# Kernel optimization log

Hardware: AMD Instinct MI355X
Metric: run time of the kernel (lower is better)

The kernel has to match this reference:

```python
import jax, jax.numpy as jnp
import numpy as np

B, N, C, H = 1, 256, 128, 4
DH = C // H  # per-head dim = 32
KEY_SCALE = DH ** -0.5


def setup_inputs() -> dict:
    key = jax.random.key(0)
    ks = jax.random.split(key, 9)
    return {
        "q_data": jax.random.normal(ks[0], (B, N, N, C), jnp.float32),
        "m_data": jax.random.normal(ks[1], (B, N, N, C), jnp.float32),
        "bias": jax.random.normal(ks[2], (B, N, 1, 1, N), jnp.float32),
        "nonbatched_bias": jax.random.normal(ks[3], (1, H, N, N), jnp.float32),
        "wq": jax.random.normal(ks[4], (C, C), jnp.float32) * (1.0 / np.sqrt(C)),
        "wk": jax.random.normal(ks[5], (C, C), jnp.float32) * (1.0 / np.sqrt(C)),
        "wv": jax.random.normal(ks[6], (C, C), jnp.float32) * (1.0 / np.sqrt(C)),
        "wo": jax.random.normal(ks[7], (C, C), jnp.float32) * (1.0 / np.sqrt(C)),
        "bo": jnp.zeros((C,), jnp.float32),
        "wg": jax.random.normal(ks[8], (C, C), jnp.float32) * (1.0 / np.sqrt(C)),
        "bg": jnp.ones((C,), jnp.float32),
    }


def reference(q_data, m_data, bias, nonbatched_bias, wq, wk, wv, wo, bo, wg, bg):
    # projections (torch Linear: x @ W.T), weights stored [out, in]
    q = (q_data @ wq.T) * KEY_SCALE            # [B, N, Nq, H*DH]
    k = m_data @ wk.T                          # [B, N, Nk, H*DH]
    v = m_data @ wv.T                          # [B, N, Nk, H*DH]
    q = q.reshape(B, N, N, H, DH)
    k = k.reshape(B, N, N, H, DH)
    v = v.reshape(B, N, N, H, DH)
    # logits: [B, N, H, Nq, Nk]
    logits = jnp.einsum("bnqhd,bnkhd->bnhqk", q, k)
    logits = logits + bias + nonbatched_bias   # bias [B,N,1,1,Nk]; nb [1,H,Nq,Nk]
    weight = jax.nn.softmax(logits, axis=-1)
    wa = jnp.einsum("bnhqk,bnkhd->bnqhd", weight, v)  # [B, N, Nq, H, DH]
    g = jax.nn.sigmoid(q_data @ wg.T + bg).reshape(B, N, N, H, DH)
    wa = wa * g
    out = wa.reshape(B, N, N, H * DH) @ wo.T + bo
    return out
```

## Files before the change

### kernel.cpp

```cpp
#include <hip/hip_runtime.h>
#include <hip/hip_bf16.h>

typedef unsigned short u16;
typedef unsigned int u32;

#define N_ 256
#define C_ 128
#define H_ 4
#define DH_ 32
#define R_ (N_*N_)

static constexpr float KEY_SCALE_ = 0.17677669529663687f;
static constexpr float LOG2E_ = 1.4426950408889634f;

typedef __attribute__((ext_vector_type(8))) short bf16x8;
typedef __attribute__((ext_vector_type(4))) float f32x4;

__device__ __forceinline__ float bf2f(u16 b){ return __uint_as_float(((u32)b)<<16); }
__device__ __forceinline__ u16 f2bf(float f){
  __hip_bfloat16 h = __float2bfloat16(f);
  u16 r; __builtin_memcpy(&r, &h, 2); return r;
}
__device__ __forceinline__ u32 pack2bf(float lo, float hi){
  __hip_bfloat162 h2 = __float22bfloat162_rn(make_float2(lo, hi));
  u32 r; __builtin_memcpy(&r, &h2, 4); return r;
}

__global__ __launch_bounds__(256) void prep_kernel(
    const float* __restrict__ wq, const float* __restrict__ wk,
    const float* __restrict__ wv, const float* __restrict__ wg,
    const float* __restrict__ nb,
    u16* __restrict__ wtb, float* __restrict__ nbT)
{
  __shared__ float T[64][65];
  const int b = blockIdx.x;
  const int t = threadIdx.x;
  if (b < 64){
    int id = b*256 + t;
    int m = id >> 12;
    int e = (id & 4095)*4;
    const float* src = (m==0) ? wq : (m==1) ? wk : (m==2) ? wv : wg;
    const float4 v = *(const float4*)(src + e);
    const float s = (m==0) ? KEY_SCALE_*LOG2E_ : 1.f;
    uint2 o;
    o.x = pack2bf(v.x*s, v.y*s);
    o.y = pack2bf(v.z*s, v.w*s);
    *(uint2*)(wtb + m*16384 + e) = o;
  } else {
    const int bb = b - 64;
    const int q0 = (bb & 3)*64, k0 = ((bb >> 2) & 3)*64;
    const int h = bb >> 4;
    const float* src = nb + (size_t)h*N_*N_;
    float* dst = nbT + (size_t)h*N_*N_;
    #pragma unroll
    for (int p=0;p<16;p++){
      int id = t + p*256;
      int r = id >> 6, cc = id & 63;
      T[cc][r] = src[(size_t)(q0 + r)*N_ + k0 + cc];
    }
    __syncthreads();
    #pragma unroll
    for (int p=0;p<16;p++){
      int id = t + p*256;
      int r = id >> 6, cc = id & 63;
      dst[(size_t)(k0 + r)*N_ + q0 + cc] = T[r][cc] * LOG2E_;
    }
  }
}

#define XSTR 136
__global__ __launch_bounds__(256, 2) void proj_kernel(
    const float* __restrict__ qd, const float* __restrict__ md,
    const u16* __restrict__ wtb, const float* __restrict__ bg,
    u16* __restrict__ qb, u16* __restrict__ kb,
    u16* __restrict__ vb, u16* __restrict__ gb)
{
  __shared__ u16 Xs[128*XSTR];
  const int t = threadIdx.x;
  const int y = blockIdx.y;
  const size_t row0 = (size_t)blockIdx.x * 128;
  const float* X = y ? md : qd;

  #pragma unroll
  for (int p=0;p<8;p++){
    int id = t + p*256;
    int r = id >> 4, c0 = (id & 15)*8;
    const float* s = X + (row0 + r)*C_ + c0;
    float4 a = *(const float4*)s;
    float4 b = *(const float4*)(s+4);
    uint2 w0; w0.x = pack2bf(a.x, a.y); w0.y = pack2bf(a.z, a.w);
    uint2 w1; w1.x = pack2bf(b.x, b.y); w1.y = pack2bf(b.z, b.w);
    *(uint2*)&Xs[r*XSTR + c0]     = w0;
    *(uint2*)&Xs[r*XSTR + c0 + 4] = w1;
  }

  const int w = t >> 6, l = t & 63, c = l & 15, g = l >> 4;
  const int matSel = w >> 1;
  const int oh = w & 1;
  const int matIdx = y ? (matSel ? 2 : 1) : (matSel ? 3 : 0);
  u16* dst = y ? (matSel ? vb : kb) : (matSel ? gb : qb);
  const bool doSig = (!y) && matSel;

  bf16x8 afr[4][4];
  {
    const u16* wb = wtb + matIdx*16384;
    #pragma unroll
    for (int ot=0;ot<4;ot++){
      const u16* rp = wb + ((oh*4+ot)*16 + c)*C_ + g*8;
      #pragma unroll
      for (int kk=0;kk<4;kk++)
        afr[ot][kk] = *(const bf16x8*)(rp + kk*32);
    }
  }
  float4 bgv[4];
  if (doSig){
    #pragma unroll
    for (int ot=0;ot<4;ot++)
      bgv[ot] = *(const float4*)&bg[(oh*4+ot)*16 + 4*g];
  }
  __syncthreads();

  for (int xt=0; xt<8; xt++){
    bf16x8 bf[4];
    #pragma unroll
    for (int kk=0;kk<4;kk++)
      bf[kk] = *(const bf16x8*)&Xs[(xt*16 + c)*XSTR + kk*32 + g*8];
    f32x4 acc[4] = {{0.f,0.f,0.f,0.f},{0.f,0.f,0.f,0.f},
                    {0.f,0.f,0.f,0.f},{0.f,0.f,0.f,0.f}};
    #pragma unroll
    for (int kk=0;kk<4;kk++){
      #pragma unroll
      for (int ot=0;ot<4;ot++)
        acc[ot] = __builtin_amdgcn_mfma_f32_16x16x32_bf16(afr[ot][kk], bf[kk], acc[ot], 0,0,0);
    }
    const size_t rowb = (row0 + xt*16 + c)*C_;
    #pragma unroll
    for (int ot=0;ot<4;ot++){
      float v0 = acc[ot][0], v1 = acc[ot][1], v2 = acc[ot][2], v3 = acc[ot][3];
      if (doSig){
        v0 = 1.f/(1.f+__expf(-(v0 + bgv[ot].x)));
        v1 = 1.f/(1.f+__expf(-(v1 + bgv[ot].y)));
        v2 = 1.f/(1.f+__expf(-(v2 + bgv[ot].z)));
        v3 = 1.f/(1.f+__expf(-(v3 + bgv[ot].w)));
      }
      uint2 pk;
      pk.x = pack2bf(v0, v1);
      pk.y = pack2bf(v2, v3);
      *(uint2*)&dst[rowb + (oh*4+ot)*16 + 4*g] = pk;
    }
  }
}

#define VSTR 264
#define OMSTR 18
__global__ __launch_bounds__(256) void attn_kernel(
    const u16* qb, const u16* __restrict__ kb,
    const u16* __restrict__ vb, const u16* __restrict__ gb,
    const float* __restrict__ bias, const float* __restrict__ nbT,
    u16* wab)
{
  __shared__ u16 Vt[32*VSTR];
  __shared__ u16 Ps[16*VSTR];
  __shared__ u32 Om[2][4][16*OMSTR];
  __shared__ float Red[2][4][16];

  const int t  = threadIdx.x;
  const int h  = blockIdx.x;
  const int n  = blockIdx.y;
  const int w  = t >> 6;
  const int l  = t & 63;
  const int c  = l & 15;
  const int g  = l >> 4;

  {
    const u16* vsrc = vb + ((size_t)n*N_)*C_ + h*DH_;
    for (int idx = t; idx < 1024; idx += 256){
      int k = idx >> 2, ch = idx & 3;
      int sk = (k & ~31) | ((k & 15) << 1) | ((k >> 4) & 1);
      ushort4 a = *(const ushort4*)(vsrc + (size_t)k*C_ + ch*8);
      ushort4 b = *(const ushort4*)(vsrc + (size_t)k*C_ + ch*8 + 4);
      u16 e[8] = {(u16)a.x,(u16)a.y,(u16)a.z,(u16)a.w,
                  (u16)b.x,(u16)b.y,(u16)b.z,(u16)b.w};
      int d0 = ch*8;
      #pragma unroll
      for (int jj=0;jj<8;jj++){
        int d = d0 + jj;
        int vr = (d&1)*16 + (d>>1);
        Vt[vr*VSTR + sk] = e[jj];
      }
    }
  }
  __syncthreads();

  bf16x8 kf[4];
  float bsv[4];
  {
    const u16* kbase = kb + ((size_t)(n*N_ + c))*C_ + h*DH_ + g*8;
    const float* brow = bias + (size_t)n*N_;
    #pragma unroll
    for (int j=0;j<4;j++){
      kf[j] = *(const bf16x8*)(kbase + (size_t)(4*w + j)*16*C_);
      bsv[j] = brow[(4*w + j)*16 + c] * LOG2E_;
    }
  }

  bf16x8 onesb;
  #pragma unroll
  for (int i=0;i<8;i++) onesb[i] = (short)0x3F80;

  const float* nbtp = nbT + (size_t)h*N_*N_;
  const u16* qbase = qb + ((size_t)(n*N_ + c))*C_ + h*DH_ + g*8;

  bf16x8 af = *(const bf16x8*)qbase;
  float4 nb4[4];
  #pragma unroll
  for (int j=0;j<4;j++)
    nb4[j] = *(const float4*)(nbtp + (size_t)((4*w+j)*16 + c)*N_ + 4*g);

  for (int it=0; it<16; ++it){
    const int p  = it & 1;
    const int q0 = it*16;

    f32x4 acc[4];
    #pragma unroll
    for (int j=0;j<4;j++){
      f32x4 ci;
      ci[0] = bsv[j] + nb4[j].x; ci[1] = bsv[j] + nb4[j].y;
      ci[2] = bsv[j] + nb4[j].z; ci[3] = bsv[j] + nb4[j].w;
      acc[j] = __builtin_amdgcn_mfma_f32_16x16x32_bf16(af, kf[j], ci, 0, 0, 0);
    }

    const int q0n = (it < 15) ? q0 + 16 : q0;
    #pragma unroll
    for (int j=0;j<4;j++)
      nb4[j] = *(const float4*)(nbtp + (size_t)((4*w+j)*16 + c)*N_ + q0n + 4*g);
    bf16x8 afn = *(const bf16x8*)(qbase + (size_t)q0n*C_);
    const size_t mrow = (size_t)n*N_ + q0 + 4*g + w;
    u32 g2 = *(const u32*)&gb[mrow*C_ + h*DH_ + 2*c];

    #pragma unroll
    for (int j=0;j<4;j++){
      #pragma unroll
      for (int r=0;r<4;r++) acc[j][r] = __builtin_amdgcn_exp2f(acc[j][r]);
    }

    #pragma unroll
    for (int r=0;r<4;r++){
      *(u32*)&Ps[(4*g+r)*VSTR + 64*w + 2*c]      = pack2bf(acc[0][r], acc[1][r]);
      *(u32*)&Ps[(4*g+r)*VSTR + 64*w + 32 + 2*c] = pack2bf(acc[2][r], acc[3][r]);
    }

    f32x4 o0 = {0.f,0.f,0.f,0.f}, o1 = {0.f,0.f,0.f,0.f};
    f32x4 o2 = {0.f,0.f,0.f,0.f};
    #pragma unroll
    for (int ss=0;ss<2;ss++){
      const int s = 2*w + ss;
      bf16x8 pa = *(const bf16x8*)&Ps[c*VSTR + s*32 + g*8];
      bf16x8 v0 = *(const bf16x8*)&Vt[(size_t)c*VSTR      + s*32 + g*8];
      bf16x8 v1 = *(const bf16x8*)&Vt[(size_t)(16+c)*VSTR + s*32 + g*8];
      o0 = __builtin_amdgcn_mfma_f32_16x16x32_bf16(pa, v0, o0, 0, 0, 0);
      o1 = __builtin_amdgcn_mfma_f32_16x16x32_bf16(pa, v1, o1, 0, 0, 0);
      o2 = __builtin_amdgcn_mfma_f32_16x16x32_bf16(pa, onesb, o2, 0, 0, 0);
    }

    if (c==0){
      #pragma unroll
      for (int r=0;r<4;r++) Red[p][w][4*g+r] = o2[r];
    }
    #pragma unroll
    for (int r=0;r<4;r++)
      Om[p][w][(4*g+r)*OMSTR + c] = pack2bf(o0[r], o1[r]);

    __syncthreads();

    {
      const int q = 4*g + w;
      float sum = (Red[p][0][q] + Red[p][1][q]) + (Red[p][2][q] + Red[p][3][q]);
      float inv = __builtin_amdgcn_rcpf(sum);
      float od0 = 0.f, od1 = 0.f;
      #pragma unroll
      for (int w2=0;w2<4;w2++){
        u32 v = Om[p][w2][q*OMSTR + c];
        od0 += bf2f((u16)(v & 0xFFFFu));
        od1 += bf2f((u16)(v >> 16));
      }
      float g0v = bf2f((u16)(g2 & 0xFFFFu));
      float g1v = bf2f((u16)(g2 >> 16));
      *(u32*)&wab[mrow*C_ + h*DH_ + 2*c] = pack2bf(od0*inv*g0v, od1*inv*g1v);
    }
    af = afn;
  }
}

#define WSTR 136
__global__ __launch_bounds__(256, 2) void outproj_kernel(
    const u16* __restrict__ wab, const float* __restrict__ wo,
    const float* __restrict__ bo, float* __restrict__ out)
{
  __shared__ u16 Wos[128*WSTR];
  const int t = threadIdx.x;
  const size_t row0 = (size_t)blockIdx.x * 128;

  #pragma unroll
  for (int p=0;p<8;p++){
    int id = t + p*256;
    int r = id >> 4, c0 = (id & 15)*8;
    const float* s = wo + r*C_ + c0;
    float4 a = *(const float4*)s;
    float4 b = *(const float4*)(s+4);
    uint2 w0; w0.x = pack2bf(a.x, a.y); w0.y = pack2bf(a.z, a.w);
    uint2 w1; w1.x = pack2bf(b.x, b.y); w1.y = pack2bf(b.z, b.w);
    *(uint2*)&Wos[r*WSTR + c0]     = w0;
    *(uint2*)&Wos[r*WSTR + c0 + 4] = w1;
  }
  __syncthreads();

  const int w = t >> 6, l = t & 63, c = l & 15, g = l >> 4;

  bf16x8 afr[2][4];
  float4 bov[2];
  #pragma unroll
  for (int ot=0;ot<2;ot++){
    #pragma unroll
    for (int kk=0;kk<4;kk++)
      afr[ot][kk] = *(const bf16x8*)&Wos[((w*2+ot)*16 + c)*WSTR + kk*32 + g*8];
    bov[ot] = *(const float4*)&bo[(w*2+ot)*16 + 4*g];
  }

  for (int xt=0; xt<8; xt++){
    bf16x8 bf[4];
    const u16* bp = wab + (row0 + xt*16 + c)*C_ + g*8;
    #pragma unroll
    for (int kk=0;kk<4;kk++)
      bf[kk] = *(const bf16x8*)(bp + kk*32);
    f32x4 acc[2] = {{0.f,0.f,0.f,0.f},{0.f,0.f,0.f,0.f}};
    #pragma unroll
    for (int kk=0;kk<4;kk++){
      #pragma unroll
      for (int ot=0;ot<2;ot++)
        acc[ot] = __builtin_amdgcn_mfma_f32_16x16x32_bf16(afr[ot][kk], bf[kk], acc[ot], 0,0,0);
    }
    const size_t rowb = (row0 + xt*16 + c)*C_;
    #pragma unroll
    for (int ot=0;ot<2;ot++){
      float4 o4;
      o4.x = acc[ot][0] + bov[ot].x;
      o4.y = acc[ot][1] + bov[ot].y;
      o4.z = acc[ot][2] + bov[ot].z;
      o4.w = acc[ot][3] + bov[ot].w;
      *(float4*)&out[rowb + (w*2+ot)*16 + 4*g] = o4;
    }
  }
}

extern "C" void kernel_launch(void* const* d_in, const int* in_sizes, int n_in,
                              void* d_out, int out_size, void* d_ws, size_t ws_size,
                              hipStream_t stream) {
  const float* qd   = (const float*)d_in[0];
  const float* md   = (const float*)d_in[1];
  const float* bias = (const float*)d_in[2];
  const float* nb   = (const float*)d_in[3];
  const float* wq   = (const float*)d_in[4];
  const float* wk   = (const float*)d_in[5];
  const float* wv   = (const float*)d_in[6];
  const float* wo   = (const float*)d_in[7];
  const float* bo   = (const float*)d_in[8];
  const float* wg   = (const float*)d_in[9];
  const float* bg   = (const float*)d_in[10];
  float* out = (float*)d_out;

  char* ws = (char*)d_ws;
  const size_t MB16 = (size_t)16*1024*1024;
  u16* qb  = (u16*)(ws);
  u16* kb  = (u16*)(ws + MB16);
  u16* vb  = (u16*)(ws + 2*MB16);
  u16* gb  = (u16*)(ws + 3*MB16);
  u16* wab = qb;
  u16*   wtb = (u16*)d_out;
  float* nbT = (float*)((char*)d_out + 131072);

  prep_kernel<<<128, 256, 0, stream>>>(wq, wk, wv, wg, nb, wtb, nbT);
  proj_kernel<<<dim3(512, 2), 256, 0, stream>>>(qd, md, wtb, bg, qb, kb, vb, gb);
  attn_kernel<<<dim3(H_, N_), 256, 0, stream>>>(qb, kb, vb, gb, bias, nbT, wab);
  outproj_kernel<<<512, 256, 0, stream>>>(wab, wo, bo, out);
}
```

Measured before the change: 103.6 us.

## Swap QK MFMA operands to keep softmax probabilities in registers, drop LDS staging

The QK^T MFMA now takes K as the A operand and Q as the B operand, so the logits come out transposed. Each lane then holds the probability values in the layout needed for the PV MFMA A operand, and they are packed straight into registers instead of going through the Ps shared-memory buffer. The V transpose swizzle is changed to match this key ordering. Because the nonbatched bias no longer needs transposing, the prep kernel just scales it in place and the bias loads become float4. This removes LDS writes and reads of P and the transpose work, at the cost of less coalesced strided bias reads and correctness that depends on the swizzle being exactly right.

```diff
diff --git a/kernel.cpp b/kernel.cpp
--- a/kernel.cpp
+++ b/kernel.cpp
@@ -30,9 +30,8 @@
     const float* __restrict__ wq, const float* __restrict__ wk,
     const float* __restrict__ wv, const float* __restrict__ wg,
     const float* __restrict__ nb,
-    u16* __restrict__ wtb, float* __restrict__ nbT)
+    u16* __restrict__ wtb, float* __restrict__ nbS)
 {
-  __shared__ float T[64][65];
   const int b = blockIdx.x;
   const int t = threadIdx.x;
   if (b < 64){
@@ -48,22 +47,14 @@
     *(uint2*)(wtb + m*16384 + e) = o;
   } else {
     const int bb = b - 64;
-    const int q0 = (bb & 3)*64, k0 = ((bb >> 2) & 3)*64;
-    const int h = bb >> 4;
-    const float* src = nb + (size_t)h*N_*N_;
-    float* dst = nbT + (size_t)h*N_*N_;
-    #pragma unroll
-    for (int p=0;p<16;p++){
-      int id = t + p*256;
-      int r = id >> 6, cc = id & 63;
-      T[cc][r] = src[(size_t)(q0 + r)*N_ + k0 + cc];
-    }
-    __syncthreads();
-    #pragma unroll
-    for (int p=0;p<16;p++){
-      int id = t + p*256;
-      int r = id >> 6, cc = id & 63;
-      dst[(size_t)(k0 + r)*N_ + q0 + cc] = T[r][cc] * LOG2E_;
+    const float4* src = (const float4*)nb;
+    float4* dst = (float4*)nbS;
+    #pragma unroll
+    for (int p=0;p<4;p++){
+      int idx = bb*1024 + p*256 + t;
+      float4 v = src[idx];
+      v.x *= LOG2E_; v.y *= LOG2E_; v.z *= LOG2E_; v.w *= LOG2E_;
+      dst[idx] = v;
     }
   }
 }
@@ -156,11 +147,10 @@
 __global__ __launch_bounds__(256) void attn_kernel(
     const u16* qb, const u16* __restrict__ kb,
     const u16* __restrict__ vb, const u16* __restrict__ gb,
-    const float* __restrict__ bias, const float* __restrict__ nbT,
+    const float* __restrict__ bias, const float* __restrict__ nbS,
     u16* wab)
 {
   __shared__ u16 Vt[32*VSTR];
-  __shared__ u16 Ps[16*VSTR];
   __shared__ u32 Om[2][4][16*OMSTR];
   __shared__ float Red[2][4][16];
 
@@ -176,7 +166,7 @@
     const u16* vsrc = vb + ((size_t)n*N_)*C_ + h*DH_;
     for (int idx = t; idx < 1024; idx += 256){
       int k = idx >> 2, ch = idx & 3;
-      int sk = (k & ~31) | ((k & 15) << 1) | ((k >> 4) & 1);
+      int sk = (k & ~63) | (k & 32) | ((k & 12) << 1) | ((k & 16) >> 2) | (k & 3);
       ushort4 a = *(const ushort4*)(vsrc + (size_t)k*C_ + ch*8);
       ushort4 b = *(const ushort4*)(vsrc + (size_t)k*C_ + ch*8 + 4);
       u16 e[8] = {(u16)a.x,(u16)a.y,(u16)a.z,(u16)a.w,
@@ -193,14 +183,15 @@
   __syncthreads();
 
   bf16x8 kf[4];
-  float bsv[4];
+  float4 bsv4[4];
   {
     const u16* kbase = kb + ((size_t)(n*N_ + c))*C_ + h*DH_ + g*8;
-    const float* brow = bias + (size_t)n*N_;
     #pragma unroll
     for (int j=0;j<4;j++){
       kf[j] = *(const bf16x8*)(kbase + (size_t)(4*w + j)*16*C_);
-      bsv[j] = brow[(4*w + j)*16 + c] * LOG2E_;
+      float4 b4 = *(const float4*)&bias[(size_t)n*N_ + (4*w+j)*16 + 4*g];
+      bsv4[j].x = b4.x*LOG2E_; bsv4[j].y = b4.y*LOG2E_;
+      bsv4[j].z = b4.z*LOG2E_; bsv4[j].w = b4.w*LOG2E_;
     }
   }
 
@@ -208,14 +199,14 @@
   #pragma unroll
   for (int i=0;i<8;i++) onesb[i] = (short)0x3F80;
 
-  const float* nbtp = nbT + (size_t)h*N_*N_;
+  const float* nbsp = nbS + (size_t)h*N_*N_;
   const u16* qbase = qb + ((size_t)(n*N_ + c))*C_ + h*DH_ + g*8;
 
   bf16x8 af = *(const bf16x8*)qbase;
   float4 nb4[4];
   #pragma unroll
   for (int j=0;j<4;j++)
-    nb4[j] = *(const float4*)(nbtp + (size_t)((4*w+j)*16 + c)*N_ + 4*g);
+    nb4[j] = *(const float4*)(nbsp + (size_t)c*N_ + (4*w+j)*16 + 4*g);
 
   for (int it=0; it<16; ++it){
     const int p  = it & 1;
@@ -225,15 +216,15 @@
     #pragma unroll
     for (int j=0;j<4;j++){
       f32x4 ci;
-      ci[0] = bsv[j] + nb4[j].x; ci[1] = bsv[j] + nb4[j].y;
-      ci[2] = bsv[j] + nb4[j].z; ci[3] = bsv[j] + nb4[j].w;
-      acc[j] = __builtin_amdgcn_mfma_f32_16x16x32_bf16(af, kf[j], ci, 0, 0, 0);
+      ci[0] = bsv4[j].x + nb4[j].x; ci[1] = bsv4[j].y + nb4[j].y;
+      ci[2] = bsv4[j].z + nb4[j].z; ci[3] = bsv4[j].w + nb4[j].w;
+      acc[j] = __builtin_amdgcn_mfma_f32_16x16x32_bf16(kf[j], af, ci, 0, 0, 0);
     }
 
     const int q0n = (it < 15) ? q0 + 16 : q0;
     #pragma unroll
     for (int j=0;j<4;j++)
-      nb4[j] = *(const float4*)(nbtp + (size_t)((4*w+j)*16 + c)*N_ + q0n + 4*g);
+      nb4[j] = *(const float4*)(nbsp + (size_t)(q0n + c)*N_ + (4*w+j)*16 + 4*g);
     bf16x8 afn = *(const bf16x8*)(qbase + (size_t)q0n*C_);
     const size_t mrow = (size_t)n*N_ + q0 + 4*g + w;
     u32 g2 = *(const u32*)&gb[mrow*C_ + h*DH_ + 2*c];
@@ -244,10 +235,15 @@
       for (int r=0;r<4;r++) acc[j][r] = __builtin_amdgcn_exp2f(acc[j][r]);
     }
 
-    #pragma unroll
-    for (int r=0;r<4;r++){
-      *(u32*)&Ps[(4*g+r)*VSTR + 64*w + 2*c]      = pack2bf(acc[0][r], acc[1][r]);
-      *(u32*)&Ps[(4*g+r)*VSTR + 64*w + 32 + 2*c] = pack2bf(acc[2][r], acc[3][r]);
+    bf16x8 pa[2];
+    #pragma unroll
+    for (int ss=0;ss<2;ss++){
+      u32 arr[4];
+      arr[0] = pack2bf(acc[2*ss][0],   acc[2*ss][1]);
+      arr[1] = pack2bf(acc[2*ss][2],   acc[2*ss][3]);
+      arr[2] = pack2bf(acc[2*ss+1][0], acc[2*ss+1][1]);
+      arr[3] = pack2bf(acc[2*ss+1][2], acc[2*ss+1][3]);
+      __builtin_memcpy(&pa[ss], arr, 16);
     }
 
     f32x4 o0 = {0.f,0.f,0.f,0.f}, o1 = {0.f,0.f,0.f,0.f};
@@ -255,12 +251,11 @@
     #pragma unroll
     for (int ss=0;ss<2;ss++){
       const int s = 2*w + ss;
-      bf16x8 pa = *(const bf16x8*)&Ps[c*VSTR + s*32 + g*8];
       bf16x8 v0 = *(const bf16x8*)&Vt[(size_t)c*VSTR      + s*32 + g*8];
       bf16x8 v1 = *(const bf16x8*)&Vt[(size_t)(16+c)*VSTR + s*32 + g*8];
-      o0 = __builtin_amdgcn_mfma_f32_16x16x32_bf16(pa, v0, o0, 0, 0, 0);
-      o1 = __builtin_amdgcn_mfma_f32_16x16x32_bf16(pa, v1, o1, 0, 0, 0);
-      o2 = __builtin_amdgcn_mfma_f32_16x16x32_bf16(pa, onesb, o2, 0, 0, 0);
+      o0 = __builtin_amdgcn_mfma_f32_16x16x32_bf16(pa[ss], v0, o0, 0, 0, 0);
+      o1 = __builtin_amdgcn_mfma_f32_16x16x32_bf16(pa[ss], v1, o1, 0, 0, 0);
+      o2 = __builtin_amdgcn_mfma_f32_16x16x32_bf16(pa[ss], onesb, o2, 0, 0, 0);
     }
 
     if (c==0){
@@ -377,10 +372,10 @@
   u16* gb  = (u16*)(ws + 3*MB16);
   u16* wab = qb;
   u16*   wtb = (u16*)d_out;
-  float* nbT = (float*)((char*)d_out + 131072);
-
-  prep_kernel<<<128, 256, 0, stream>>>(wq, wk, wv, wg, nb, wtb, nbT);
+  float* nbS = (float*)((char*)d_out + 131072);
+
+  prep_kernel<<<128, 256, 0, stream>>>(wq, wk, wv, wg, nb, wtb, nbS);
   proj_kernel<<<dim3(512, 2), 256, 0, stream>>>(qd, md, wtb, bg, qb, kb, vb, gb);
-  attn_kernel<<<dim3(H_, N_), 256, 0, stream>>>(qb, kb, vb, gb, bias, nbT, wab);
+  attn_kernel<<<dim3(H_, N_), 256, 0, stream>>>(qb, kb, vb, gb, bias, nbS, wab);
   outproj_kernel<<<512, 256, 0, stream>>>(wab, wo, bo, out);
 }
```

New measurement: 101.9 us, median of 2. About the same (-1.6%).
